# Kernel optimization log

Hardware: AMD Instinct MI355X
Metric: run time of the kernel (lower is better)

The kernel has to match this reference:

```python
import jax, jax.numpy as jnp
import numpy as np

WS = 8        # window_size
NH = 12       # num_heads


def setup_inputs() -> dict:
    key = jax.random.key(0)
    ks = jax.random.split(key, 9)
    B, C, H, W = 4, 384, 128, 128
    s = 1.0 / np.sqrt(C)
    x = jax.random.normal(ks[0], (B, C, H, W), dtype=jnp.float32)
    Wq = jax.random.normal(ks[1], (C, C), dtype=jnp.float32) * s
    bq = jax.random.normal(ks[2], (C,), dtype=jnp.float32) * 0.01
    Wk = jax.random.normal(ks[3], (C, C), dtype=jnp.float32) * s
    bk = jax.random.normal(ks[4], (C,), dtype=jnp.float32) * 0.01
    Wv = jax.random.normal(ks[5], (C, C), dtype=jnp.float32) * s
    bv = jax.random.normal(ks[6], (C,), dtype=jnp.float32) * 0.01
    Wp = jax.random.normal(ks[7], (C, C), dtype=jnp.float32) * s
    bp = jax.random.normal(ks[8], (C,), dtype=jnp.float32) * 0.01
    return {"x": x, "Wq": Wq, "bq": bq, "Wk": Wk, "bk": bk,
            "Wv": Wv, "bv": bv, "Wp": Wp, "bp": bp}


def reference(x, Wq, bq, Wk, bk, Wv, bv, Wp, bp):
    B, C, H, W = x.shape
    ws2 = WS * WS
    dk = C // NH
    scale = dk ** -0.5

    # window_partition: flat row-major reshape (same semantics as torch's
    # reshape on a contiguous [B,C,H,W] tensor), then permute+view.
    p = x.reshape(B, H // WS, WS, W // WS, WS, C)
    p = jnp.transpose(p, (0, 5, 1, 3, 2, 4))          # [B, C, H/ws, W/ws, ws, ws]
    p = p.reshape(B, C, -1, ws2)                       # [B, C, nW, ws*ws]

    def conv1x1(w, b):  # 1x1 Conv2d on [B,C,nW,ws2]
        return jnp.einsum('bcnw,oc->bonw', p, w) + b[None, :, None, None]

    def heads(t):  # permute(0,2,3,1).contiguous().reshape -> [B, NH, nW, ws2, dk]
        t = jnp.transpose(t, (0, 2, 3, 1))             # [B, nW, ws2, C]
        return t.reshape(B, NH, -1, ws2, dk)           # row-major reinterpretation

    q = heads(conv1x1(Wq, bq))
    k = heads(conv1x1(Wk, bk))
    v = heads(conv1x1(Wv, bv))

    scores = jnp.einsum('bhnqd,bhnkd->bhnqk', q, k) * scale
    attn = jax.nn.softmax(scores, axis=-1)
    o = jnp.einsum('bhnqk,bhnkd->bhnqd', attn, v)      # [B, NH, nW, ws2, dk]
    o = o.reshape(B, -1, ws2, C)                       # [B, nW, ws2, C]

    # window_unpartition
    u = o.reshape(B, -1, WS, WS, C)
    u = jnp.transpose(u, (0, 4, 1, 2, 3))              # [B, C, nW, ws, ws]
    u = u.reshape(B, C, H, W)

    y = jnp.einsum('bchw,oc->bohw', u, Wp) + bp[None, :, None, None]
    return y
```

## Files before the change

kernel.cpp:

```cpp
#include <hip/hip_runtime.h>
#include <hip/hip_bf16.h>
#include <stdint.h>


typedef __bf16 bf16_t;
typedef __bf16 bf16x8 __attribute__((ext_vector_type(8)));
typedef __bf16 bf16x4 __attribute__((ext_vector_type(4)));
typedef float f32x4 __attribute__((ext_vector_type(4)));

__device__ __forceinline__ void gload_lds16(const void* g, void* l) {
  __builtin_amdgcn_global_load_lds((__attribute__((address_space(1))) void*)(g),
                                   (__attribute__((address_space(3))) void*)(l),
                                   16, 0, 0);
}

__global__ __launch_bounds__(256) void convw_kernel(
    const float* __restrict__ wq, const float* __restrict__ wk,
    const float* __restrict__ wv, const float* __restrict__ wp,
    bf16_t* __restrict__ oq, bf16_t* __restrict__ ok,
    bf16_t* __restrict__ ov, bf16_t* __restrict__ op_) {
  int i = blockIdx.x * 256 + threadIdx.x;
  oq[i] = (bf16_t)wq[i];
  ok[i] = (bf16_t)wk[i];
  ov[i] = (bf16_t)wv[i];
  op_[i] = (bf16_t)wp[i];
}

__global__ __launch_bounds__(256) void prep_kernel(const float* __restrict__ x,
                                                   bf16_t* __restrict__ Xp) {
  int gid = blockIdx.x * 256 + threadIdx.x;
  int row = gid / 96;
  int c4 = (gid - row * 96) * 4;
  int b = row >> 14;
  int pp = row & 16383;
  int n1 = pp >> 10, n3 = (pp >> 6) & 15, w2 = (pp >> 3) & 7, w4 = pp & 7;
  int P = (n1 << 10) | (w2 << 7) | (n3 << 3) | w4;
  float4 v = *(const float4*)(x + (size_t)((b << 14) | P) * 384 + c4);
  bf16x4 o;
  o[0] = (bf16_t)v.x; o[1] = (bf16_t)v.y; o[2] = (bf16_t)v.z; o[3] = (bf16_t)v.w;
  *(bf16x4*)(Xp + (size_t)row * 384 + c4) = o;
}

__global__ __launch_bounds__(512, 4) void qkv_gemm(
    const bf16_t* __restrict__ Xp, const bf16_t* __restrict__ Wcat,
    const float* __restrict__ bq, const float* __restrict__ bk,
    const float* __restrict__ bv,
    bf16_t* __restrict__ Qs, bf16_t* __restrict__ Ks, bf16_t* __restrict__ Vs) {
  extern __shared__ __align__(16) char smem[];
  const int tid = threadIdx.x;
  const int F = blockIdx.x;
  const int xcd = F & 7;
  const int t = F >> 3;
  const int j = t % 9;
  const int gq = t / 9;
  const int m0 = (gq * 8 + xcd) * 256;
  const int which = j / 3;
  const int cb = (j % 3) * 128;
  const float* bias = which == 0 ? bq : (which == 1 ? bk : bv);
  bf16_t* Out = which == 0 ? Qs : (which == 1 ? Ks : Vs);
  const bf16_t* Arows = Xp + (size_t)m0 * 384;
  const bf16_t* Brows = Wcat + (size_t)j * 128 * 384;

  const int lane = tid & 63, wid = tid >> 6;
  const int l15 = lane & 15, hi = lane >> 4;
  const int wr = wid >> 1, wc = wid & 1;
  const int slot = hi ^ ((l15 >> 1) & 3);

  auto stage = [&](int kt) {
    const int k0 = kt * 32;
    char* base = smem + (kt % 3) * 24576;
#pragma unroll
    for (int jj = 0; jj < 2; ++jj) {
      int idx = jj * 512 + tid;
      int row = idx >> 2;
      int sg = (idx & 3) ^ ((idx >> 3) & 3);
      gload_lds16(Arows + (size_t)row * 384 + k0 + sg * 8,
                  base + (jj * 512 + wid * 64) * 16);
    }
    {
      int row = tid >> 2;
      int sg = (tid & 3) ^ ((tid >> 3) & 3);
      gload_lds16(Brows + (size_t)row * 384 + k0 + sg * 8,
                  base + 16384 + (wid * 64) * 16);
    }
  };

  stage(0); stage(1);
  asm volatile("s_waitcnt vmcnt(3)" ::: "memory");
  __builtin_amdgcn_s_barrier();
  __builtin_amdgcn_sched_barrier(0);

  f32x4 acc[4][4] = {};
#pragma unroll
  for (int kt = 0; kt < 12; ++kt) {
    if (kt > 0) {
      __builtin_amdgcn_s_barrier();
      __builtin_amdgcn_sched_barrier(0);
    }
    if (kt + 2 < 12) stage(kt + 2);
    const char* Ab = smem + (kt % 3) * 24576;
    const char* Bb = Ab + 16384;
    bf16x8 a[4], bfr[4];
#pragma unroll
    for (int i = 0; i < 4; ++i)
      a[i] = *(const bf16x8*)(Ab + (wr * 64 + i * 16 + l15) * 64 + slot * 16);
#pragma unroll
    for (int ni = 0; ni < 4; ++ni)
      bfr[ni] = *(const bf16x8*)(Bb + (wc * 64 + ni * 16 + l15) * 64 + slot * 16);
    __builtin_amdgcn_s_setprio(1);
#pragma unroll
    for (int mi = 0; mi < 4; ++mi)
#pragma unroll
      for (int ni = 0; ni < 4; ++ni)
        acc[mi][ni] = __builtin_amdgcn_mfma_f32_16x16x32_bf16(a[mi], bfr[ni],
                                                              acc[mi][ni], 0, 0, 0);
    __builtin_amdgcn_s_setprio(0);
    if (kt <= 9)       asm volatile("s_waitcnt vmcnt(3)" ::: "memory");
    else if (kt == 10) asm volatile("s_waitcnt vmcnt(0)" ::: "memory");
    __builtin_amdgcn_sched_barrier(0);
  }

#pragma unroll
  for (int ni = 0; ni < 4; ++ni) {
    int chan = cb + wc * 64 + ni * 16 + l15;
    float bv_ = bias[chan];
#pragma unroll
    for (int mi = 0; mi < 4; ++mi)
#pragma unroll
      for (int r = 0; r < 4; ++r) {
        int row = m0 + wr * 64 + mi * 16 + hi * 4 + r;
        Out[(size_t)row * 384 + chan] = (bf16_t)(acc[mi][ni][r] + bv_);
      }
  }
}

__global__ __launch_bounds__(64) void attn_kernel(const bf16_t* __restrict__ Q,
                                                  const bf16_t* __restrict__ K,
                                                  const bf16_t* __restrict__ V,
                                                  bf16_t* __restrict__ O) {
  const size_t base = (size_t)blockIdx.x * 2048;
  const bf16_t* q = Q + base;
  const bf16_t* k = K + base;
  const bf16_t* v = V + base;
  bf16_t* o = O + base;
  const int lane = threadIdx.x;
  const int l15 = lane & 15, hi = lane >> 4;

  __shared__ __align__(16) bf16_t Vt[32][72];
  __shared__ __align__(16) bf16_t Ps[64][72];

#pragma unroll
  for (int j = 0; j < 4; ++j) {
    bf16x8 vv = *(const bf16x8*)(v + lane * 32 + j * 8);
#pragma unroll
    for (int e = 0; e < 8; ++e) Vt[j * 8 + e][lane] = vv[e];
  }

  bf16x8 aQ[4], bK[4];
#pragma unroll
  for (int i = 0; i < 4; ++i) {
    aQ[i] = *(const bf16x8*)(q + (i * 16 + l15) * 32 + hi * 8);
    bK[i] = *(const bf16x8*)(k + (i * 16 + l15) * 32 + hi * 8);
  }
  f32x4 sc[4][4] = {};
#pragma unroll
  for (int mi = 0; mi < 4; ++mi)
#pragma unroll
    for (int ni = 0; ni < 4; ++ni)
      sc[mi][ni] = __builtin_amdgcn_mfma_f32_16x16x32_bf16(aQ[mi], bK[ni],
                                                           sc[mi][ni], 0, 0, 0);

  const float SCALE = 0.17677669529663687f;
  float rs[4][4];
#pragma unroll
  for (int mi = 0; mi < 4; ++mi) {
#pragma unroll
    for (int r = 0; r < 4; ++r) {
      float s0 = sc[mi][0][r] * SCALE, s1 = sc[mi][1][r] * SCALE;
      float s2 = sc[mi][2][r] * SCALE, s3 = sc[mi][3][r] * SCALE;
      float mx = fmaxf(fmaxf(s0, s1), fmaxf(s2, s3));
      mx = fmaxf(mx, __shfl_xor(mx, 1));
      mx = fmaxf(mx, __shfl_xor(mx, 2));
      mx = fmaxf(mx, __shfl_xor(mx, 4));
      mx = fmaxf(mx, __shfl_xor(mx, 8));
      float p0 = __expf(s0 - mx), p1 = __expf(s1 - mx);
      float p2 = __expf(s2 - mx), p3 = __expf(s3 - mx);
      int row = mi * 16 + hi * 4 + r;
      Ps[row][0 + l15] = (bf16_t)p0;
      Ps[row][16 + l15] = (bf16_t)p1;
      Ps[row][32 + l15] = (bf16_t)p2;
      Ps[row][48 + l15] = (bf16_t)p3;
      float sum = p0 + p1 + p2 + p3;
      sum += __shfl_xor(sum, 1);
      sum += __shfl_xor(sum, 2);
      sum += __shfl_xor(sum, 4);
      sum += __shfl_xor(sum, 8);
      rs[mi][r] = sum;
    }
  }
  __syncthreads();

  f32x4 oacc[4][2] = {};
#pragma unroll
  for (int mi = 0; mi < 4; ++mi)
#pragma unroll
    for (int ks = 0; ks < 2; ++ks) {
      bf16x8 aP = *(const bf16x8*)(&Ps[mi * 16 + l15][ks * 32 + hi * 8]);
#pragma unroll
      for (int n2 = 0; n2 < 2; ++n2) {
        bf16x8 bV = *(const bf16x8*)(&Vt[n2 * 16 + l15][ks * 32 + hi * 8]);
        oacc[mi][n2] = __builtin_amdgcn_mfma_f32_16x16x32_bf16(aP, bV,
                                                               oacc[mi][n2], 0, 0, 0);
      }
    }
#pragma unroll
  for (int mi = 0; mi < 4; ++mi)
#pragma unroll
    for (int n2 = 0; n2 < 2; ++n2)
#pragma unroll
      for (int r = 0; r < 4; ++r) {
        int row = mi * 16 + hi * 4 + r;
        o[row * 32 + n2 * 16 + l15] = (bf16_t)(oacc[mi][n2][r] / rs[mi][r]);
      }
}

__device__ __forceinline__ void stage_tile(const bf16_t* __restrict__ A,
                                           const bf16_t* __restrict__ B,
                                           bf16_t* As, bf16_t* Bs, int k0, int tid) {
  const int lane = tid & 63, wvv = tid >> 6;
  const int s = (lane & 3) ^ ((lane >> 3) & 3);
#pragma unroll
  for (int j = 0; j < 2; ++j) {
    int q = wvv * 128 + j * 64 + lane;
    int row = q >> 2;
    gload_lds16(A + (size_t)row * 384 + k0 + s * 8,
                (char*)As + (wvv * 128 + j * 64) * 16);
    gload_lds16(B + (size_t)row * 384 + k0 + s * 8,
                (char*)Bs + (wvv * 128 + j * 64) * 16);
  }
}

__device__ __forceinline__ void gemm_mainloop(const bf16_t* __restrict__ Arows,
                                              const bf16_t* __restrict__ Brows,
                                              bf16_t* As, bf16_t* Bs,
                                              int tid, f32x4 acc[4][4]) {
  const int lane = tid & 63;
  const int l15 = lane & 15, hi = lane >> 4;
  const int wr = (tid >> 6) >> 1, wc = (tid >> 6) & 1;
  const int slot = hi ^ ((l15 >> 1) & 3);
  stage_tile(Arows, Brows, As, Bs, 0, tid);
  stage_tile(Arows, Brows, As + 4096, Bs + 4096, 32, tid);
#pragma unroll
  for (int kt = 0; kt < 12; ++kt) {
    bf16_t* Ab = As + (kt & 1) * 4096;
    bf16_t* Bb = Bs + (kt & 1) * 4096;
    if (kt == 11) asm volatile("s_waitcnt vmcnt(0)" ::: "memory");
    else          asm volatile("s_waitcnt vmcnt(4)" ::: "memory");
    __builtin_amdgcn_s_barrier();
    bf16x8 a[4], bfr[4];
#pragma unroll
    for (int i = 0; i < 4; ++i) {
      a[i] = *(const bf16x8*)(Ab + (wr * 64 + i * 16 + l15) * 32 + slot * 8);
      bfr[i] = *(const bf16x8*)(Bb + (wc * 64 + i * 16 + l15) * 32 + slot * 8);
    }
#pragma unroll
    for (int mi = 0; mi < 4; ++mi)
#pragma unroll
      for (int ni = 0; ni < 4; ++ni)
        acc[mi][ni] = __builtin_amdgcn_mfma_f32_16x16x32_bf16(a[mi], bfr[ni],
                                                              acc[mi][ni], 0, 0, 0);
    asm volatile("s_waitcnt lgkmcnt(0)" ::: "memory");
    __builtin_amdgcn_sched_barrier(0);
    __builtin_amdgcn_s_barrier();
    if (kt + 2 < 12)
      stage_tile(Arows, Brows, Ab, Bb, (kt + 2) * 32, tid);
  }
}

__global__ __launch_bounds__(256) void proj_gemm(const bf16_t* __restrict__ Wpb,
                                                 const bf16_t* __restrict__ O,
                                                 const float* __restrict__ bp,
                                                 float* __restrict__ y) {
  __shared__ __align__(16) bf16_t As[2 * 128 * 32];
  __shared__ __align__(16) bf16_t Bs[2 * 128 * 32];
  const int tid = threadIdx.x;
  const int F = blockIdx.x;
  const int xcd = F & 7;
  const int t = F >> 3;
  const int j = t % 3;
  const int gq = t / 3;
  const int g = gq * 8 + xcd;
  const int n0 = (g & 127) * 128;
  const int b = g >> 7;
  const int m0 = j * 128;
  f32x4 acc[4][4] = {};
  gemm_mainloop(Wpb + (size_t)m0 * 384, O + ((size_t)b * 16384 + n0) * 384,
                As, Bs, tid, acc);
  const int lane = tid & 63, wvv = tid >> 6;
  const int l15 = lane & 15, hi = lane >> 4;
  const int wr = wvv >> 1, wc = wvv & 1;
  float* yb = y + (size_t)b * 6291456;
#pragma unroll
  for (int mi = 0; mi < 4; ++mi)
#pragma unroll
    for (int r = 0; r < 4; ++r) {
      int och = m0 + wr * 64 + mi * 16 + hi * 4 + r;
      float bpv = bp[och];
#pragma unroll
      for (int ni = 0; ni < 4; ++ni) {
        int pix = n0 + wc * 64 + ni * 16 + l15;
        yb[(size_t)och * 16384 + pix] = acc[mi][ni][r] + bpv;
      }
    }
}

extern "C" void kernel_launch(void* const* d_in, const int* in_sizes, int n_in,
                              void* d_out, int out_size, void* d_ws, size_t ws_size,
                              hipStream_t stream) {
  const float* x  = (const float*)d_in[0];
  const float* Wq = (const float*)d_in[1];
  const float* bq = (const float*)d_in[2];
  const float* Wk = (const float*)d_in[3];
  const float* bk = (const float*)d_in[4];
  const float* Wv = (const float*)d_in[5];
  const float* bv = (const float*)d_in[6];
  const float* Wp = (const float*)d_in[7];
  const float* bp = (const float*)d_in[8];
  float* y = (float*)d_out;

  char* ws = (char*)d_ws;
  const size_t SZ = 50331648;
  bf16_t* Xp  = (bf16_t*)(ws);
  bf16_t* Vs  = (bf16_t*)(ws + SZ);
  bf16_t* Wcat = (bf16_t*)(ws + 2 * SZ);
  bf16_t* Wkb = Wcat + 147456;
  bf16_t* Wvb = Wkb + 147456;
  bf16_t* Wpb = Wvb + 147456;
  bf16_t* Qs  = (bf16_t*)d_out;
  bf16_t* Ks  = (bf16_t*)((char*)d_out + SZ);
  bf16_t* Ob  = Xp;

  hipFuncSetAttribute((const void*)qkv_gemm,
                      hipFuncAttributeMaxDynamicSharedMemorySize, 73728);

  convw_kernel<<<576, 256, 0, stream>>>(Wq, Wk, Wv, Wp, Wcat, Wkb, Wvb, Wpb);
  prep_kernel<<<24576, 256, 0, stream>>>(x, Xp);
  qkv_gemm<<<2304, 512, 73728, stream>>>(Xp, Wcat, bq, bk, bv, Qs, Ks, Vs);
  attn_kernel<<<12288, 64, 0, stream>>>(Qs, Ks, Vs, Ob);
  proj_gemm<<<1536, 256, 0, stream>>>(Wpb, Ob, bp, y);
}
```

Before: 187.3 us.

## Shrink QKV GEMM tiles, unify proj GEMM pipeline, merge prep kernels

Merges the weight-conversion and input-prep kernels into a single launch, which saves one launch and its gap. The QKV GEMM tile drops from 256x128 to 128x128 with 8 waves in a 2x4 layout, doubling the grid and cutting LDS per block so more blocks fit per CU. The projection GEMM is rewritten to use the same 512-thread, triple-buffered, 128x128 pipeline as the QKV GEMM. Smaller tiles mean less operand reuse per block and more global traffic, traded for higher occupancy and better load balance.

```diff
diff --git a/kernel.cpp b/kernel.cpp
--- a/kernel.cpp
+++ b/kernel.cpp
@@ -14,21 +14,21 @@
                                    16, 0, 0);
 }
 
-__global__ __launch_bounds__(256) void convw_kernel(
+__global__ __launch_bounds__(256) void prepw_kernel(
+    const float* __restrict__ x, bf16_t* __restrict__ Xp,
     const float* __restrict__ wq, const float* __restrict__ wk,
     const float* __restrict__ wv, const float* __restrict__ wp,
     bf16_t* __restrict__ oq, bf16_t* __restrict__ ok,
     bf16_t* __restrict__ ov, bf16_t* __restrict__ op_) {
-  int i = blockIdx.x * 256 + threadIdx.x;
-  oq[i] = (bf16_t)wq[i];
-  ok[i] = (bf16_t)wk[i];
-  ov[i] = (bf16_t)wv[i];
-  op_[i] = (bf16_t)wp[i];
-}
-
-__global__ __launch_bounds__(256) void prep_kernel(const float* __restrict__ x,
-                                                   bf16_t* __restrict__ Xp) {
-  int gid = blockIdx.x * 256 + threadIdx.x;
+  if (blockIdx.x < 576) {
+    int i = blockIdx.x * 256 + threadIdx.x;
+    oq[i] = (bf16_t)wq[i];
+    ok[i] = (bf16_t)wk[i];
+    ov[i] = (bf16_t)wv[i];
+    op_[i] = (bf16_t)wp[i];
+    return;
+  }
+  int gid = (blockIdx.x - 576) * 256 + threadIdx.x;
   int row = gid / 96;
   int c4 = (gid - row * 96) * 4;
   int b = row >> 14;
@@ -41,7 +41,7 @@
   *(bf16x4*)(Xp + (size_t)row * 384 + c4) = o;
 }
 
-__global__ __launch_bounds__(512, 4) void qkv_gemm(
+__global__ __launch_bounds__(512, 6) void qkv_gemm(
     const bf16_t* __restrict__ Xp, const bf16_t* __restrict__ Wcat,
     const float* __restrict__ bq, const float* __restrict__ bk,
     const float* __restrict__ bv,
@@ -53,7 +53,7 @@
   const int t = F >> 3;
   const int j = t % 9;
   const int gq = t / 9;
-  const int m0 = (gq * 8 + xcd) * 256;
+  const int m0 = (gq * 8 + xcd) * 128;
   const int which = j / 3;
   const int cb = (j % 3) * 128;
   const float* bias = which == 0 ? bq : (which == 1 ? bk : bv);
@@ -63,34 +63,32 @@
 
   const int lane = tid & 63, wid = tid >> 6;
   const int l15 = lane & 15, hi = lane >> 4;
-  const int wr = wid >> 1, wc = wid & 1;
+  const int wr = wid >> 2, wc = wid & 3;
   const int slot = hi ^ ((l15 >> 1) & 3);
 
   auto stage = [&](int kt) {
     const int k0 = kt * 32;
-    char* base = smem + (kt % 3) * 24576;
-#pragma unroll
-    for (int jj = 0; jj < 2; ++jj) {
-      int idx = jj * 512 + tid;
-      int row = idx >> 2;
-      int sg = (idx & 3) ^ ((idx >> 3) & 3);
+    char* base = smem + (kt % 3) * 16384;
+    {
+      int row = tid >> 2;
+      int sg = (tid & 3) ^ ((tid >> 3) & 3);
       gload_lds16(Arows + (size_t)row * 384 + k0 + sg * 8,
-                  base + (jj * 512 + wid * 64) * 16);
+                  base + (wid * 64) * 16);
     }
     {
       int row = tid >> 2;
       int sg = (tid & 3) ^ ((tid >> 3) & 3);
       gload_lds16(Brows + (size_t)row * 384 + k0 + sg * 8,
-                  base + 16384 + (wid * 64) * 16);
+                  base + 8192 + (wid * 64) * 16);
     }
   };
 
   stage(0); stage(1);
-  asm volatile("s_waitcnt vmcnt(3)" ::: "memory");
+  asm volatile("s_waitcnt vmcnt(2)" ::: "memory");
   __builtin_amdgcn_s_barrier();
   __builtin_amdgcn_sched_barrier(0);
 
-  f32x4 acc[4][4] = {};
+  f32x4 acc[4][2] = {};
 #pragma unroll
   for (int kt = 0; kt < 12; ++kt) {
     if (kt > 0) {
@@ -98,31 +96,31 @@
       __builtin_amdgcn_sched_barrier(0);
     }
     if (kt + 2 < 12) stage(kt + 2);
-    const char* Ab = smem + (kt % 3) * 24576;
-    const char* Bb = Ab + 16384;
-    bf16x8 a[4], bfr[4];
+    const char* Ab = smem + (kt % 3) * 16384;
+    const char* Bb = Ab + 8192;
+    bf16x8 a[4], bfr[2];
 #pragma unroll
     for (int i = 0; i < 4; ++i)
       a[i] = *(const bf16x8*)(Ab + (wr * 64 + i * 16 + l15) * 64 + slot * 16);
 #pragma unroll
-    for (int ni = 0; ni < 4; ++ni)
-      bfr[ni] = *(const bf16x8*)(Bb + (wc * 64 + ni * 16 + l15) * 64 + slot * 16);
+    for (int ni = 0; ni < 2; ++ni)
+      bfr[ni] = *(const bf16x8*)(Bb + (wc * 32 + ni * 16 + l15) * 64 + slot * 16);
     __builtin_amdgcn_s_setprio(1);
 #pragma unroll
     for (int mi = 0; mi < 4; ++mi)
 #pragma unroll
-      for (int ni = 0; ni < 4; ++ni)
+      for (int ni = 0; ni < 2; ++ni)
         acc[mi][ni] = __builtin_amdgcn_mfma_f32_16x16x32_bf16(a[mi], bfr[ni],
                                                               acc[mi][ni], 0, 0, 0);
     __builtin_amdgcn_s_setprio(0);
-    if (kt <= 9)       asm volatile("s_waitcnt vmcnt(3)" ::: "memory");
+    if (kt <= 9)       asm volatile("s_waitcnt vmcnt(2)" ::: "memory");
     else if (kt == 10) asm volatile("s_waitcnt vmcnt(0)" ::: "memory");
     __builtin_amdgcn_sched_barrier(0);
   }
 
 #pragma unroll
-  for (int ni = 0; ni < 4; ++ni) {
-    int chan = cb + wc * 64 + ni * 16 + l15;
+  for (int ni = 0; ni < 2; ++ni) {
+    int chan = cb + wc * 32 + ni * 16 + l15;
     float bv_ = bias[chan];
 #pragma unroll
     for (int mi = 0; mi < 4; ++mi)
@@ -224,65 +222,10 @@
       }
 }
 
-__device__ __forceinline__ void stage_tile(const bf16_t* __restrict__ A,
-                                           const bf16_t* __restrict__ B,
-                                           bf16_t* As, bf16_t* Bs, int k0, int tid) {
-  const int lane = tid & 63, wvv = tid >> 6;
-  const int s = (lane & 3) ^ ((lane >> 3) & 3);
-#pragma unroll
-  for (int j = 0; j < 2; ++j) {
-    int q = wvv * 128 + j * 64 + lane;
-    int row = q >> 2;
-    gload_lds16(A + (size_t)row * 384 + k0 + s * 8,
-                (char*)As + (wvv * 128 + j * 64) * 16);
-    gload_lds16(B + (size_t)row * 384 + k0 + s * 8,
-                (char*)Bs + (wvv * 128 + j * 64) * 16);
-  }
-}
-
-__device__ __forceinline__ void gemm_mainloop(const bf16_t* __restrict__ Arows,
-                                              const bf16_t* __restrict__ Brows,
-                                              bf16_t* As, bf16_t* Bs,
-                                              int tid, f32x4 acc[4][4]) {
-  const int lane = tid & 63;
-  const int l15 = lane & 15, hi = lane >> 4;
-  const int wr = (tid >> 6) >> 1, wc = (tid >> 6) & 1;
-  const int slot = hi ^ ((l15 >> 1) & 3);
-  stage_tile(Arows, Brows, As, Bs, 0, tid);
-  stage_tile(Arows, Brows, As + 4096, Bs + 4096, 32, tid);
-#pragma unroll
-  for (int kt = 0; kt < 12; ++kt) {
-    bf16_t* Ab = As + (kt & 1) * 4096;
-    bf16_t* Bb = Bs + (kt & 1) * 4096;
-    if (kt == 11) asm volatile("s_waitcnt vmcnt(0)" ::: "memory");
-    else          asm volatile("s_waitcnt vmcnt(4)" ::: "memory");
-    __builtin_amdgcn_s_barrier();
-    bf16x8 a[4], bfr[4];
-#pragma unroll
-    for (int i = 0; i < 4; ++i) {
-      a[i] = *(const bf16x8*)(Ab + (wr * 64 + i * 16 + l15) * 32 + slot * 8);
-      bfr[i] = *(const bf16x8*)(Bb + (wc * 64 + i * 16 + l15) * 32 + slot * 8);
-    }
-#pragma unroll
-    for (int mi = 0; mi < 4; ++mi)
-#pragma unroll
-      for (int ni = 0; ni < 4; ++ni)
-        acc[mi][ni] = __builtin_amdgcn_mfma_f32_16x16x32_bf16(a[mi], bfr[ni],
-                                                              acc[mi][ni], 0, 0, 0);
-    asm volatile("s_waitcnt lgkmcnt(0)" ::: "memory");
-    __builtin_amdgcn_sched_barrier(0);
-    __builtin_amdgcn_s_barrier();
-    if (kt + 2 < 12)
-      stage_tile(Arows, Brows, Ab, Bb, (kt + 2) * 32, tid);
-  }
-}
-
-__global__ __launch_bounds__(256) void proj_gemm(const bf16_t* __restrict__ Wpb,
-                                                 const bf16_t* __restrict__ O,
-                                                 const float* __restrict__ bp,
-                                                 float* __restrict__ y) {
-  __shared__ __align__(16) bf16_t As[2 * 128 * 32];
-  __shared__ __align__(16) bf16_t Bs[2 * 128 * 32];
+__global__ __launch_bounds__(512, 6) void proj_gemm(
+    const bf16_t* __restrict__ Wpb, const bf16_t* __restrict__ O,
+    const float* __restrict__ bp, float* __restrict__ y) {
+  extern __shared__ __align__(16) char smem[];
   const int tid = threadIdx.x;
   const int F = blockIdx.x;
   const int xcd = F & 7;
@@ -293,12 +236,60 @@
   const int n0 = (g & 127) * 128;
   const int b = g >> 7;
   const int m0 = j * 128;
-  f32x4 acc[4][4] = {};
-  gemm_mainloop(Wpb + (size_t)m0 * 384, O + ((size_t)b * 16384 + n0) * 384,
-                As, Bs, tid, acc);
-  const int lane = tid & 63, wvv = tid >> 6;
+  const bf16_t* Arows = Wpb + (size_t)m0 * 384;
+  const bf16_t* Brows = O + ((size_t)b * 16384 + n0) * 384;
+
+  const int lane = tid & 63, wid = tid >> 6;
   const int l15 = lane & 15, hi = lane >> 4;
-  const int wr = wvv >> 1, wc = wvv & 1;
+  const int wr = wid >> 2, wc = wid & 3;
+  const int slot = hi ^ ((l15 >> 1) & 3);
+
+  auto stage = [&](int kt) {
+    const int k0 = kt * 32;
+    char* base = smem + (kt % 3) * 16384;
+    int row = tid >> 2;
+    int sg = (tid & 3) ^ ((tid >> 3) & 3);
+    gload_lds16(Arows + (size_t)row * 384 + k0 + sg * 8,
+                base + (wid * 64) * 16);
+    gload_lds16(Brows + (size_t)row * 384 + k0 + sg * 8,
+                base + 8192 + (wid * 64) * 16);
+  };
+
+  stage(0); stage(1);
+  asm volatile("s_waitcnt vmcnt(2)" ::: "memory");
+  __builtin_amdgcn_s_barrier();
+  __builtin_amdgcn_sched_barrier(0);
+
+  f32x4 acc[4][2] = {};
+#pragma unroll
+  for (int kt = 0; kt < 12; ++kt) {
+    if (kt > 0) {
+      __builtin_amdgcn_s_barrier();
+      __builtin_amdgcn_sched_barrier(0);
+    }
+    if (kt + 2 < 12) stage(kt + 2);
+    const char* Ab = smem + (kt % 3) * 16384;
+    const char* Bb = Ab + 8192;
+    bf16x8 a[4], bfr[2];
+#pragma unroll
+    for (int i = 0; i < 4; ++i)
+      a[i] = *(const bf16x8*)(Ab + (wr * 64 + i * 16 + l15) * 64 + slot * 16);
+#pragma unroll
+    for (int ni = 0; ni < 2; ++ni)
+      bfr[ni] = *(const bf16x8*)(Bb + (wc * 32 + ni * 16 + l15) * 64 + slot * 16);
+    __builtin_amdgcn_s_setprio(1);
+#pragma unroll
+    for (int mi = 0; mi < 4; ++mi)
+#pragma unroll
+      for (int ni = 0; ni < 2; ++ni)
+        acc[mi][ni] = __builtin_amdgcn_mfma_f32_16x16x32_bf16(a[mi], bfr[ni],
+                                                              acc[mi][ni], 0, 0, 0);
+    __builtin_amdgcn_s_setprio(0);
+    if (kt <= 9)       asm volatile("s_waitcnt vmcnt(2)" ::: "memory");
+    else if (kt == 10) asm volatile("s_waitcnt vmcnt(0)" ::: "memory");
+    __builtin_amdgcn_sched_barrier(0);
+  }
+
   float* yb = y + (size_t)b * 6291456;
 #pragma unroll
   for (int mi = 0; mi < 4; ++mi)
@@ -307,8 +298,8 @@
       int och = m0 + wr * 64 + mi * 16 + hi * 4 + r;
       float bpv = bp[och];
 #pragma unroll
-      for (int ni = 0; ni < 4; ++ni) {
-        int pix = n0 + wc * 64 + ni * 16 + l15;
+      for (int ni = 0; ni < 2; ++ni) {
+        int pix = n0 + wc * 32 + ni * 16 + l15;
         yb[(size_t)och * 16384 + pix] = acc[mi][ni][r] + bpv;
       }
     }
@@ -340,12 +331,9 @@
   bf16_t* Ks  = (bf16_t*)((char*)d_out + SZ);
   bf16_t* Ob  = Xp;
 
-  hipFuncSetAttribute((const void*)qkv_gemm,
-                      hipFuncAttributeMaxDynamicSharedMemorySize, 73728);
-
-  convw_kernel<<<576, 256, 0, stream>>>(Wq, Wk, Wv, Wp, Wcat, Wkb, Wvb, Wpb);
-  prep_kernel<<<24576, 256, 0, stream>>>(x, Xp);
-  qkv_gemm<<<2304, 512, 73728, stream>>>(Xp, Wcat, bq, bk, bv, Qs, Ks, Vs);
+  prepw_kernel<<<25152, 256, 0, stream>>>(x, Xp, Wq, Wk, Wv, Wp,
+                                          Wcat, Wkb, Wvb, Wpb);
+  qkv_gemm<<<4608, 512, 49152, stream>>>(Xp, Wcat, bq, bk, bv, Qs, Ks, Vs);
   attn_kernel<<<12288, 64, 0, stream>>>(Qs, Ks, Vs, Ob);
-  proj_gemm<<<1536, 256, 0, stream>>>(Wpb, Ob, bp, y);
-}
+  proj_gemm<<<1536, 512, 49152, stream>>>(Wpb, Ob, bp, y);
+}
```

New measurement: 183.3 us, median of 3. 1.02x faster.
